# Kernel optimization log

Measured on AMD Instinct MI355X. Metric: run time of the kernel, lower is better.

## Reference

```python
import jax, jax.numpy as jnp
import numpy as np

B, S, D = 8, 2048, 2048
E, R, K = 8, 16, 2
NUM_TASKS, NUM_MODES = 4, 2
ALPHA = 16.0


def setup_inputs() -> dict:
    key = jax.random.key(0)
    k1, k2, k3, k4 = jax.random.split(key, 4)
    hidden_states = jax.random.normal(k1, (B, S, D), dtype=jnp.float32)
    gate_w = jax.random.normal(k2, (E, D), dtype=jnp.float32) * 0.01  # nn.init.normal_(std=0.01)
    # Soft-prior biases: fill(-1.0), strong prior 3.0 / 2.0 at configured (task, expert) / (mode, expert)
    tb = -np.ones((NUM_TASKS, E), dtype=np.float32)
    mb = -np.ones((NUM_MODES, E), dtype=np.float32)
    for e in range(E):
        tb[e % NUM_TASKS, e] = 3.0
        mb[e % NUM_MODES, e] = 2.0
    # LoRA params; lora_B is zero-init in torch but we use small random values for a nontrivial baseline
    lora_A = jax.random.normal(k3, (E, R, D), dtype=jnp.float32) * (1.0 / np.sqrt(D))
    lora_B = jax.random.normal(k4, (E, D, R), dtype=jnp.float32) * 0.02
    return {
        "hidden_states": hidden_states,
        "gate_w": gate_w,
        "task_bias": jnp.asarray(tb),
        "mode_bias": jnp.asarray(mb),
        "lora_A": lora_A,
        "lora_B": lora_B,
        "task_id": 1,
        "mode_id": 1,
    }


def reference(hidden_states, gate_w, task_bias, mode_bias, lora_A, lora_B, task_id, mode_id):
    scaling = ALPHA / R
    # Router: score = dynamic_gate(mean_pool(x)) + task_bias[t] + mode_bias[m]
    x_pooled = hidden_states.mean(axis=1)                       # [B, D]
    logits = x_pooled @ gate_w.T + task_bias[task_id] + mode_bias[mode_id]  # [B, E]
    top_v, top_i = jax.lax.top_k(logits, K)                     # [B, K]
    weights = jax.nn.softmax(top_v, axis=-1)                    # [B, K]
    # per-sample, per-expert combine weight: sum of top-k weights routed to that expert
    one_hot = jax.nn.one_hot(top_i, E, dtype=weights.dtype)     # [B, K, E]
    sw = jnp.einsum('bke,bk->be', one_hot, weights)             # [B, E]
    # LoRA experts: (x @ A_e^T) @ B_e^T * scaling, weighted-summed per sample
    mid = jnp.einsum('bsd,erd->besr', hidden_states, lora_A)    # [B, E, S, R] (small: R=16)
    out = jnp.einsum('be,besr,edr->bsd', sw, mid, lora_B) * scaling  # [B, S, D]
    return out
```

## Files before the change

### kernel.cpp

```cpp
#include <hip/hip_runtime.h>
#include <stdint.h>

typedef __attribute__((ext_vector_type(8))) short bf16x8;
typedef __attribute__((ext_vector_type(4))) float f32x4;
typedef __attribute__((ext_vector_type(16))) float f32x16;
typedef unsigned short ushort_t;

#define B_ 8
#define S_ 2048
#define D_ 2048
#define E_ 8
#define J_ 128
#define M_ 32
#define AROWS 136
#define ATILE (AROWS * 64)

static __device__ __forceinline__ unsigned short f2bf(float f) {
  union { float f; uint32_t u; } v; v.f = f;
  uint32_t u = v.u;
  return (unsigned short)((u + 0x7FFFu + ((u >> 16) & 1u)) >> 16);
}
static __device__ __forceinline__ float bf2f(ushort_t h) {
  union { uint32_t u; float f; } v; v.u = ((uint32_t)h) << 16;
  return v.f;
}
static __device__ __forceinline__ uint32_t pkbf(float a, float b) {
  uint32_t r;
  asm("v_cvt_pk_bf16_f32 %0, %1, %2" : "=v"(r) : "v"(a), "v"(b));
  return r;
}

#define GLL16(gsrc, ldst)                                                        \
  __builtin_amdgcn_global_load_lds(                                              \
      (const __attribute__((address_space(1))) void*)(gsrc),                     \
      (__attribute__((address_space(3))) void*)(ldst), 16, 0, 0)

#define SBAR() __builtin_amdgcn_sched_barrier(0)
#define VMWAIT(N)                                                                \
  do {                                                                           \
    asm volatile("s_waitcnt vmcnt(" #N ")" ::: "memory");                        \
    __builtin_amdgcn_sched_barrier(0);                                           \
  } while (0)
#define VMBAR(N)                                                                 \
  do {                                                                           \
    asm volatile("s_waitcnt vmcnt(" #N ") lgkmcnt(0)\n\ts_barrier" ::: "memory");\
    __builtin_amdgcn_sched_barrier(0);                                           \
  } while (0)

__global__ void k_prep(const float* __restrict__ lA, const float* __restrict__ lB,
                       const float* __restrict__ gw,
                       ushort_t* __restrict__ AgE, ushort_t* __restrict__ Bg) {
  int gid = blockIdx.x * blockDim.x + threadIdx.x;
  int stride = gridDim.x * blockDim.x;
  for (int o = gid; o < 32 * AROWS * 8; o += stride) {
    int kt = o / (AROWS * 8);
    int rem = o - kt * (AROWS * 8);
    int row = rem >> 3, c = rem & 7;
    int d = kt * 64 + (((c ^ row) & 7) << 3);
    const float* src = (row < 128) ? (lA + (size_t)row * D_ + d)
                                   : (gw + (size_t)(row - 128) * D_ + d);
    float4 v0 = *(const float4*)src;
    float4 v1 = *(const float4*)(src + 4);
    bf16x8 outv;
    outv[0] = (short)f2bf(v0.x); outv[1] = (short)f2bf(v0.y);
    outv[2] = (short)f2bf(v0.z); outv[3] = (short)f2bf(v0.w);
    outv[4] = (short)f2bf(v1.x); outv[5] = (short)f2bf(v1.y);
    outv[6] = (short)f2bf(v1.z); outv[7] = (short)f2bf(v1.w);
    *(bf16x8*)&AgE[(size_t)o * 8] = outv;
  }
  for (int o4 = gid; o4 < (D_ * J_) / 4; o4 += stride) {
    int j4 = o4 & 31, dd = o4 >> 5;
    int e = j4 >> 2, r0 = (j4 & 3) * 4;
    float4 v = *(const float4*)(lB + ((size_t)e * D_ + dd) * 16 + r0);
    uint2 pk;
    pk.x = (uint32_t)f2bf(v.x) | ((uint32_t)f2bf(v.y) << 16);
    pk.y = (uint32_t)f2bf(v.z) | ((uint32_t)f2bf(v.w) << 16);
    ((uint2*)Bg)[o4] = pk;
  }
}

__global__ __launch_bounds__(256, 2) void k_mid(const float* __restrict__ x,
    const ushort_t* __restrict__ AgE, ushort_t* __restrict__ midb,
    float* __restrict__ lpart) {
  __shared__ ushort_t Ab[3][ATILE];
  __shared__ ushort_t Xb[2][M_ * 64];
  const int tid = threadIdx.x;
  const int w = tid >> 6, lane = tid & 63;
  const int l31 = lane & 31, hi = lane >> 5;
  const int jp = w & 1, xi = w >> 1;
  const int b = blockIdx.y, s0 = blockIdx.x * M_;
  const int xr = tid >> 3, xc = (tid & 7) * 8;
  const float* xsrc = x + ((size_t)(b * S_ + s0 + xr)) * D_ + xc;
  const int xwoff = xr * 64 + (((tid & 7) ^ (xr & 7)) << 3);

  f32x16 accA = {}, accB = {}, acc2 = {};

  auto stageA = [&](int buf, int kt) {
#pragma unroll
    for (int c = 0; c < 4; ++c) {
      int ch = c * 256 + tid;
      GLL16(AgE + (size_t)kt * ATILE + (size_t)ch * 8, &Ab[buf][ch * 8]);
    }
    {
      int ch = 1024 + lane;
      GLL16(AgE + (size_t)kt * ATILE + (size_t)ch * 8, &Ab[buf][(1024 + lane) * 8]);
    }
  };
  auto loadX = [&](float4* r4, int t) {
    const float* p = xsrc + t * 64;
    r4[0] = *(const float4*)(p);
    r4[1] = *(const float4*)(p + 4);
  };
  auto cvtWrite = [&](int buf, const float4* r4) {
    uint4 q;
    q.x = pkbf(r4[0].x, r4[0].y); q.y = pkbf(r4[0].z, r4[0].w);
    q.z = pkbf(r4[1].x, r4[1].y); q.w = pkbf(r4[1].z, r4[1].w);
    *(uint4*)&Xb[buf][xwoff] = q;
  };
  auto computeTile = [&](int t, int ab) {
    const int xbuf = t & 1;
    const int a0 = jp * 64 + l31, a1 = jp * 64 + 32 + l31, a2 = 128 + l31;
    const int rsw = (l31 & 7);
#pragma unroll
    for (int k2 = 0; k2 < 2; ++k2) {
      const int ks = xi * 2 + k2;
      const int cc = ks * 2 + hi;
      const int chs = ((cc ^ rsw) << 3);
      bf16x8 xf = *(const bf16x8*)&Xb[xbuf][l31 * 64 + chs];
      bf16x8 af0 = *(const bf16x8*)&Ab[ab][a0 * 64 + chs];
      bf16x8 af1 = *(const bf16x8*)&Ab[ab][a1 * 64 + chs];
      accA = __builtin_amdgcn_mfma_f32_32x32x16_bf16(af0, xf, accA, 0, 0, 0);
      accB = __builtin_amdgcn_mfma_f32_32x32x16_bf16(af1, xf, accB, 0, 0, 0);
      if (jp == 0) {
        bf16x8 af2 = *(const bf16x8*)&Ab[ab][a2 * 64 + chs];
        acc2 = __builtin_amdgcn_mfma_f32_32x32x16_bf16(af2, xf, acc2, 0, 0, 0);
      }
    }
  };

  float4 xS0[2], xS1[2];
  loadX(xS0, 0); SBAR();
  stageA(0, 0);  SBAR();
  loadX(xS1, 1); SBAR();
  stageA(1, 1);  SBAR();
  VMWAIT(12);
  cvtWrite(0, xS0);
  VMBAR(7);

#define BODY(T, AB, ABN, XCUR, XNXT)                                             \
  do {                                                                           \
    loadX(XNXT, (T) + 2); SBAR();                                                \
    stageA((ABN), (T) + 2); SBAR();                                              \
    computeTile((T), (AB));                                                      \
    VMWAIT(12);                                                                  \
    cvtWrite(((T) + 1) & 1, XCUR);                                               \
    VMBAR(7);                                                                    \
  } while (0)

#pragma unroll 1
  for (int k6 = 0; k6 < 5; ++k6) {
    const int t0 = 6 * k6;
    BODY(t0 + 0, 0, 2, xS1, xS0);
    BODY(t0 + 1, 1, 0, xS0, xS1);
    BODY(t0 + 2, 2, 1, xS1, xS0);
    BODY(t0 + 3, 0, 2, xS0, xS1);
    BODY(t0 + 4, 1, 0, xS1, xS0);
    BODY(t0 + 5, 2, 1, xS0, xS1);
  }
#undef BODY
  computeTile(30, 0);
  VMWAIT(5);
  cvtWrite(1, xS1);
  VMBAR(0);
  computeTile(31, 1);

  __syncthreads();
  float* scr  = (float*)&Ab[0][0];
  float* scr2 = (float*)&Ab[1][0];
  if (xi == 1) {
    float* p = scr + ((size_t)(jp * 64 + lane)) * 32;
#pragma unroll
    for (int G = 0; G < 4; ++G) {
      f32x4 tA, tB;
      tA[0] = accA[G * 4 + 0]; tA[1] = accA[G * 4 + 1];
      tA[2] = accA[G * 4 + 2]; tA[3] = accA[G * 4 + 3];
      tB[0] = accB[G * 4 + 0]; tB[1] = accB[G * 4 + 1];
      tB[2] = accB[G * 4 + 2]; tB[3] = accB[G * 4 + 3];
      *(f32x4*)&p[G * 4]      = tA;
      *(f32x4*)&p[16 + G * 4] = tB;
    }
    if (jp == 0) {
      float* p2 = scr2 + lane * 4;
      p2[0] = acc2[0]; p2[1] = acc2[1]; p2[2] = acc2[2]; p2[3] = acc2[3];
    }
  }
  __syncthreads();
  if (xi == 0) {
    const float* p = scr + ((size_t)(jp * 64 + lane)) * 32;
#pragma unroll
    for (int i = 0; i < 16; ++i) { accA[i] += p[i]; accB[i] += p[16 + i]; }
    ushort_t* mp = midb + ((size_t)(b * S_ + s0 + l31)) * J_ + jp * 64 + 4 * hi;
#pragma unroll
    for (int G = 0; G < 4; ++G) {
      uint2 pA, pB;
      pA.x = pkbf(accA[G * 4 + 0], accA[G * 4 + 1]);
      pA.y = pkbf(accA[G * 4 + 2], accA[G * 4 + 3]);
      pB.x = pkbf(accB[G * 4 + 0], accB[G * 4 + 1]);
      pB.y = pkbf(accB[G * 4 + 2], accB[G * 4 + 3]);
      *(uint2*)&mp[G * 8] = pA;
      *(uint2*)&mp[32 + G * 8] = pB;
    }
    if (jp == 0) {
      const float* p2 = scr2 + lane * 4;
#pragma unroll
      for (int q = 0; q < 4; ++q) {
        float v = acc2[q] + p2[q];
        v += __shfl_xor(v, 1); v += __shfl_xor(v, 2);
        v += __shfl_xor(v, 4); v += __shfl_xor(v, 8);
        v += __shfl_xor(v, 16);
        if (l31 == 0)
          lpart[((size_t)(b * 64 + blockIdx.x)) * 8 + hi * 4 + q] = v;
      }
    }
  }
}

__global__ void k_router(const float* __restrict__ lpart,
                         const float* __restrict__ tb, const float* __restrict__ mb,
                         const int* __restrict__ task_p, const int* __restrict__ mode_p,
                         float* __restrict__ rinfo) {
  __shared__ float lg[64];
  const int t = threadIdx.x;
  const int b = t >> 3, e = t & 7;
  float s = 0.f;
  for (int k = 0; k < 64; ++k) s += lpart[((size_t)(b * 64 + k)) * 8 + e];
  lg[t] = s * (1.f / (float)S_) + tb[task_p[0] * E_ + e] + mb[mode_p[0] * E_ + e];
  __syncthreads();
  if (t < B_) {
    float v[8];
#pragma unroll
    for (int e2 = 0; e2 < 8; ++e2) v[e2] = lg[t * 8 + e2];
    int i1 = 0;
#pragma unroll
    for (int e2 = 1; e2 < 8; ++e2) if (v[e2] > v[i1]) i1 = e2;
    int i2 = (i1 == 0) ? 1 : 0;
#pragma unroll
    for (int e2 = 0; e2 < 8; ++e2) if (e2 != i1 && v[e2] > v[i2]) i2 = e2;
    float ex = __expf(v[i2] - v[i1]);
    float w1 = 1.f / (1.f + ex), w2 = ex * w1;
    float4 r;
    r.x = (float)i1; r.y = (float)i2; r.z = w1; r.w = w2;
    ((float4*)rinfo)[t] = r;
  }
}

__global__ __launch_bounds__(256) void k_comb(const ushort_t* __restrict__ midb,
    const float* __restrict__ rinfo, const ushort_t* __restrict__ Bg,
    float* __restrict__ out) {
  __shared__ ushort_t Bt[128][40];
  const int n = blockIdx.x, m = blockIdx.y, b = blockIdx.z;
  const int tid = threadIdx.x, w = tid >> 6, lane = tid & 63;
  const int lm = lane & 15, g = lane >> 4;

  const float4 ri = ((const float4*)rinfo)[b];
  const int i1 = (int)ri.x, i2 = (int)ri.y;
  const float w1 = ri.z, w2 = ri.w;

#pragma unroll
  for (int c = 0; c < 2; ++c) {
    int ci = c * 256 + tid;
    int d = ci >> 2, sub = ci & 3;
    int e = (sub & 2) ? i2 : i1;
    float sc = (sub & 2) ? w2 : w1;
    bf16x8 bv = *(const bf16x8*)(Bg + ((size_t)(n * 128 + d)) * J_ + e * 16 + (sub & 1) * 8);
    bf16x8 bw;
#pragma unroll
    for (int i = 0; i < 8; ++i) bw[i] = (short)f2bf(bf2f((ushort_t)bv[i]) * sc);
    *(bf16x8*)&Bt[d][sub * 8] = bw;
  }

  const int srow = m * 64 + w * 16 + lm;
  const int jw = (g < 2) ? (i1 * 16 + g * 8) : (i2 * 16 + (g - 2) * 8);
  bf16x8 pf = *(const bf16x8*)&midb[((size_t)(b * S_ + srow)) * J_ + jw];
  __syncthreads();

  f32x4 acc[8] = {};
#pragma unroll
  for (int nn = 0; nn < 8; ++nn) {
    bf16x8 af = *(const bf16x8*)&Bt[nn * 16 + lm][g * 8];
    acc[nn] = __builtin_amdgcn_mfma_f32_16x16x32_bf16(af, pf, acc[nn], 0, 0, 0);
  }

  float* op = out + ((size_t)(b * S_ + srow)) * D_ + n * 128;
#pragma unroll
  for (int nn = 0; nn < 8; ++nn)
    *(f32x4*)&op[nn * 16 + g * 4] = acc[nn];
}

extern "C" void kernel_launch(void* const* d_in, const int* in_sizes, int n_in,
                              void* d_out, int out_size, void* d_ws, size_t ws_size,
                              hipStream_t stream) {
  const float* x    = (const float*)d_in[0];
  const float* gw   = (const float*)d_in[1];
  const float* tb   = (const float*)d_in[2];
  const float* mb   = (const float*)d_in[3];
  const float* lA   = (const float*)d_in[4];
  const float* lB   = (const float*)d_in[5];
  const int* task_p = (const int*)d_in[6];
  const int* mode_p = (const int*)d_in[7];
  float* out = (float*)d_out;
  char* ws = (char*)d_ws;
  ushort_t* midb = (ushort_t*)ws;
  ushort_t* AgE  = (ushort_t*)(ws + 4194304);
  ushort_t* Bg   = (ushort_t*)(ws + 4751360);
  float* lpart   = (float*)(ws + 5275648);
  float* rinfo   = (float*)(ws + 5292032);

  hipLaunchKernelGGL(k_prep, dim3(256), dim3(256), 0, stream, lA, lB, gw, AgE, Bg);
  hipLaunchKernelGGL(k_mid, dim3(64, 8), dim3(256), 0, stream, x, AgE, midb, lpart);
  hipLaunchKernelGGL(k_router, dim3(1), dim3(64), 0, stream,
                     lpart, tb, mb, task_p, mode_p, rinfo);
  hipLaunchKernelGGL(k_comb, dim3(16, 32, 8), dim3(256), 0, stream, midb, rinfo, Bg, out);
}
```

Measured before the change: 84.20 us.

## Double k_mid row tile to 64 with 512-thread blocks and 4-way K split

The mid-projection kernel now handles 64 sequence rows per block using 8 waves. Each wave computes a 2x2 grid of MFMA tiles, so every A-fragment load from LDS is reused across two X fragments, and the four K-slices are reduced through LDS in three rounds. The X tile swizzle is changed to suit the larger tile. Block count is halved, to 256 blocks, which cuts repeated staging of the LoRA-A and gate tiles. In exchange it adds more accumulator registers, a longer serialized reduction, and fewer blocks to spread across the CUs.

New measurement: 76.57 us. 9.1% less time.

```diff
diff --git a/kernel.cpp b/kernel.cpp
--- a/kernel.cpp
+++ b/kernel.cpp
@@ -11,7 +11,7 @@
 #define D_ 2048
 #define E_ 8
 #define J_ 128
-#define M_ 32
+#define M_ 64
 #define AROWS 136
 #define ATILE (AROWS * 64)
 
@@ -28,6 +28,9 @@
   uint32_t r;
   asm("v_cvt_pk_bf16_f32 %0, %1, %2" : "=v"(r) : "v"(a), "v"(b));
   return r;
+}
+static __device__ __forceinline__ int xswz(int row) {
+  return (row & 7) ^ (((row >> 3) & 3) << 1);
 }
 
 #define GLL16(gsrc, ldst)                                                        \
@@ -56,7 +59,7 @@
     int kt = o / (AROWS * 8);
     int rem = o - kt * (AROWS * 8);
     int row = rem >> 3, c = rem & 7;
-    int d = kt * 64 + (((c ^ row) & 7) << 3);
+    int d = kt * 64 + (((c ^ xswz(row)) & 7) << 3);
     const float* src = (row < 128) ? (lA + (size_t)row * D_ + d)
                                    : (gw + (size_t)(row - 128) * D_ + d);
     float4 v0 = *(const float4*)src;
@@ -79,32 +82,29 @@
   }
 }
 
-__global__ __launch_bounds__(256, 2) void k_mid(const float* __restrict__ x,
+__global__ __launch_bounds__(512, 2) void k_mid(const float* __restrict__ x,
     const ushort_t* __restrict__ AgE, ushort_t* __restrict__ midb,
     float* __restrict__ lpart) {
   __shared__ ushort_t Ab[3][ATILE];
-  __shared__ ushort_t Xb[2][M_ * 64];
+  __shared__ ushort_t Xb[2][4096];
+  __shared__ float lsc[4][8];
   const int tid = threadIdx.x;
   const int w = tid >> 6, lane = tid & 63;
   const int l31 = lane & 31, hi = lane >> 5;
-  const int jp = w & 1, xi = w >> 1;
+  const int jp = w & 1, xk = w >> 1;
   const int b = blockIdx.y, s0 = blockIdx.x * M_;
-  const int xr = tid >> 3, xc = (tid & 7) * 8;
-  const float* xsrc = x + ((size_t)(b * S_ + s0 + xr)) * D_ + xc;
-  const int xwoff = xr * 64 + (((tid & 7) ^ (xr & 7)) << 3);
-
-  f32x16 accA = {}, accB = {}, acc2 = {};
+  const int xr = tid >> 3;
+  const float* xsrc = x + ((size_t)(b * S_ + s0 + xr)) * D_ + (tid & 7) * 8;
+  const int xwoff = xr * 64 + ((((tid & 7) ^ xswz(xr)) & 7) << 3);
+  const int Xs = xswz(l31);
+
+  f32x16 acc00 = {}, acc01 = {}, acc10 = {}, acc11 = {}, acc2 = {};
 
   auto stageA = [&](int buf, int kt) {
-#pragma unroll
-    for (int c = 0; c < 4; ++c) {
-      int ch = c * 256 + tid;
-      GLL16(AgE + (size_t)kt * ATILE + (size_t)ch * 8, &Ab[buf][ch * 8]);
-    }
-    {
-      int ch = 1024 + lane;
-      GLL16(AgE + (size_t)kt * ATILE + (size_t)ch * 8, &Ab[buf][(1024 + lane) * 8]);
-    }
+    const ushort_t* base = AgE + (size_t)kt * ATILE;
+    GLL16(base + (size_t)tid * 8, &Ab[buf][tid * 8]);
+    GLL16(base + (size_t)(512 + tid) * 8, &Ab[buf][(512 + tid) * 8]);
+    GLL16(base + (size_t)(1024 + lane) * 8, &Ab[buf][(1024 + lane) * 8]);
   };
   auto loadX = [&](float4* r4, int t) {
     const float* p = xsrc + t * 64;
@@ -118,23 +118,22 @@
     *(uint4*)&Xb[buf][xwoff] = q;
   };
   auto computeTile = [&](int t, int ab) {
-    const int xbuf = t & 1;
-    const int a0 = jp * 64 + l31, a1 = jp * 64 + 32 + l31, a2 = 128 + l31;
-    const int rsw = (l31 & 7);
-#pragma unroll
-    for (int k2 = 0; k2 < 2; ++k2) {
-      const int ks = xi * 2 + k2;
-      const int cc = ks * 2 + hi;
-      const int chs = ((cc ^ rsw) << 3);
-      bf16x8 xf = *(const bf16x8*)&Xb[xbuf][l31 * 64 + chs];
-      bf16x8 af0 = *(const bf16x8*)&Ab[ab][a0 * 64 + chs];
-      bf16x8 af1 = *(const bf16x8*)&Ab[ab][a1 * 64 + chs];
-      accA = __builtin_amdgcn_mfma_f32_32x32x16_bf16(af0, xf, accA, 0, 0, 0);
-      accB = __builtin_amdgcn_mfma_f32_32x32x16_bf16(af1, xf, accB, 0, 0, 0);
-      if (jp == 0) {
-        bf16x8 af2 = *(const bf16x8*)&Ab[ab][a2 * 64 + chs];
-        acc2 = __builtin_amdgcn_mfma_f32_32x32x16_bf16(af2, xf, acc2, 0, 0, 0);
-      }
+    const int cc = xk * 2 + hi;
+    const int chs = (((cc ^ Xs) & 7) << 3);
+    const ushort_t* Xp = &Xb[t & 1][l31 * 64 + chs];
+    bf16x8 xf0 = *(const bf16x8*)Xp;
+    bf16x8 xf1 = *(const bf16x8*)(Xp + 2048);
+    const ushort_t* Ap = &Ab[ab][(jp * 64 + l31) * 64 + chs];
+    bf16x8 af0 = *(const bf16x8*)Ap;
+    bf16x8 af1 = *(const bf16x8*)(Ap + 2048);
+    acc00 = __builtin_amdgcn_mfma_f32_32x32x16_bf16(af0, xf0, acc00, 0, 0, 0);
+    acc10 = __builtin_amdgcn_mfma_f32_32x32x16_bf16(af0, xf1, acc10, 0, 0, 0);
+    acc01 = __builtin_amdgcn_mfma_f32_32x32x16_bf16(af1, xf0, acc01, 0, 0, 0);
+    acc11 = __builtin_amdgcn_mfma_f32_32x32x16_bf16(af1, xf1, acc11, 0, 0, 0);
+    if (jp == 0) {
+      bf16x8 af2 = *(const bf16x8*)&Ab[ab][(128 + l31) * 64 + chs];
+      acc2 = __builtin_amdgcn_mfma_f32_32x32x16_bf16(af2, xf0, acc2, 0, 0, 0);
+      acc2 = __builtin_amdgcn_mfma_f32_32x32x16_bf16(af2, xf1, acc2, 0, 0, 0);
     }
   };
 
@@ -143,18 +142,18 @@
   stageA(0, 0);  SBAR();
   loadX(xS1, 1); SBAR();
   stageA(1, 1);  SBAR();
-  VMWAIT(12);
+  VMWAIT(8);
   cvtWrite(0, xS0);
-  VMBAR(7);
+  VMBAR(5);
 
 #define BODY(T, AB, ABN, XCUR, XNXT)                                             \
   do {                                                                           \
     loadX(XNXT, (T) + 2); SBAR();                                                \
     stageA((ABN), (T) + 2); SBAR();                                              \
     computeTile((T), (AB));                                                      \
-    VMWAIT(12);                                                                  \
+    VMWAIT(8);                                                                   \
     cvtWrite(((T) + 1) & 1, XCUR);                                               \
-    VMBAR(7);                                                                    \
+    VMBAR(5);                                                                    \
   } while (0)
 
 #pragma unroll 1
@@ -169,59 +168,78 @@
   }
 #undef BODY
   computeTile(30, 0);
-  VMWAIT(5);
+  VMWAIT(3);
   cvtWrite(1, xS1);
   VMBAR(0);
   computeTile(31, 1);
 
   __syncthreads();
-  float* scr  = (float*)&Ab[0][0];
-  float* scr2 = (float*)&Ab[1][0];
-  if (xi == 1) {
-    float* p = scr + ((size_t)(jp * 64 + lane)) * 32;
-#pragma unroll
-    for (int G = 0; G < 4; ++G) {
-      f32x4 tA, tB;
-      tA[0] = accA[G * 4 + 0]; tA[1] = accA[G * 4 + 1];
-      tA[2] = accA[G * 4 + 2]; tA[3] = accA[G * 4 + 3];
-      tB[0] = accB[G * 4 + 0]; tB[1] = accB[G * 4 + 1];
-      tB[2] = accB[G * 4 + 2]; tB[3] = accB[G * 4 + 3];
-      *(f32x4*)&p[G * 4]      = tA;
-      *(f32x4*)&p[16 + G * 4] = tB;
-    }
-    if (jp == 0) {
-      float* p2 = scr2 + lane * 4;
-      p2[0] = acc2[0]; p2[1] = acc2[1]; p2[2] = acc2[2]; p2[3] = acc2[3];
+
+  if (jp == 0) {
+#pragma unroll
+    for (int q = 0; q < 4; ++q) {
+      float v = acc2[q];
+      v += __shfl_xor(v, 1); v += __shfl_xor(v, 2); v += __shfl_xor(v, 4);
+      v += __shfl_xor(v, 8); v += __shfl_xor(v, 16);
+      if (l31 == 0) lsc[xk][hi * 4 + q] = v;
+    }
+  }
+
+  float* const reg0 = (float*)&Ab[0][0];
+  float* const reg1 = (float*)&Ab[1][0];
+#pragma unroll 1
+  for (int r = 1; r <= 3; ++r) {
+    __syncthreads();
+    if (xk == r) {
+      float* p = jp ? reg1 : reg0;
+#pragma unroll
+      for (int i = 0; i < 16; ++i) {
+        p[i * 64 + lane]        = acc00[i];
+        p[(16 + i) * 64 + lane] = acc01[i];
+        p[(32 + i) * 64 + lane] = acc10[i];
+        p[(48 + i) * 64 + lane] = acc11[i];
+      }
+    }
+    __syncthreads();
+    if (xk == 0) {
+      const float* p = jp ? reg1 : reg0;
+#pragma unroll
+      for (int i = 0; i < 16; ++i) {
+        acc00[i] += p[i * 64 + lane];
+        acc01[i] += p[(16 + i) * 64 + lane];
+        acc10[i] += p[(32 + i) * 64 + lane];
+        acc11[i] += p[(48 + i) * 64 + lane];
+      }
     }
   }
   __syncthreads();
-  if (xi == 0) {
-    const float* p = scr + ((size_t)(jp * 64 + lane)) * 32;
-#pragma unroll
-    for (int i = 0; i < 16; ++i) { accA[i] += p[i]; accB[i] += p[16 + i]; }
-    ushort_t* mp = midb + ((size_t)(b * S_ + s0 + l31)) * J_ + jp * 64 + 4 * hi;
-#pragma unroll
-    for (int G = 0; G < 4; ++G) {
-      uint2 pA, pB;
-      pA.x = pkbf(accA[G * 4 + 0], accA[G * 4 + 1]);
-      pA.y = pkbf(accA[G * 4 + 2], accA[G * 4 + 3]);
-      pB.x = pkbf(accB[G * 4 + 0], accB[G * 4 + 1]);
-      pB.y = pkbf(accB[G * 4 + 2], accB[G * 4 + 3]);
-      *(uint2*)&mp[G * 8] = pA;
-      *(uint2*)&mp[32 + G * 8] = pB;
-    }
-    if (jp == 0) {
-      const float* p2 = scr2 + lane * 4;
-#pragma unroll
-      for (int q = 0; q < 4; ++q) {
-        float v = acc2[q] + p2[q];
-        v += __shfl_xor(v, 1); v += __shfl_xor(v, 2);
-        v += __shfl_xor(v, 4); v += __shfl_xor(v, 8);
-        v += __shfl_xor(v, 16);
-        if (l31 == 0)
-          lpart[((size_t)(b * 64 + blockIdx.x)) * 8 + hi * 4 + q] = v;
+
+  if (xk == 0) {
+#pragma unroll
+    for (int sp = 0; sp < 2; ++sp) {
+      ushort_t* mp = midb + ((size_t)(b * S_ + s0 + sp * 32 + l31)) * J_ + jp * 64 + 4 * hi;
+#pragma unroll
+      for (int G = 0; G < 4; ++G) {
+        uint2 pA, pB;
+        if (sp == 0) {
+          pA.x = pkbf(acc00[G * 4 + 0], acc00[G * 4 + 1]);
+          pA.y = pkbf(acc00[G * 4 + 2], acc00[G * 4 + 3]);
+          pB.x = pkbf(acc01[G * 4 + 0], acc01[G * 4 + 1]);
+          pB.y = pkbf(acc01[G * 4 + 2], acc01[G * 4 + 3]);
+        } else {
+          pA.x = pkbf(acc10[G * 4 + 0], acc10[G * 4 + 1]);
+          pA.y = pkbf(acc10[G * 4 + 2], acc10[G * 4 + 3]);
+          pB.x = pkbf(acc11[G * 4 + 0], acc11[G * 4 + 1]);
+          pB.y = pkbf(acc11[G * 4 + 2], acc11[G * 4 + 3]);
+        }
+        *(uint2*)&mp[G * 8] = pA;
+        *(uint2*)&mp[32 + G * 8] = pB;
       }
     }
+  }
+  if (w == 0 && lane < 8) {
+    float s = lsc[0][lane] + lsc[1][lane] + lsc[2][lane] + lsc[3][lane];
+    lpart[((size_t)(b * 32 + blockIdx.x)) * 8 + lane] = s;
   }
 }
 
@@ -233,7 +251,7 @@
   const int t = threadIdx.x;
   const int b = t >> 3, e = t & 7;
   float s = 0.f;
-  for (int k = 0; k < 64; ++k) s += lpart[((size_t)(b * 64 + k)) * 8 + e];
+  for (int k = 0; k < 32; ++k) s += lpart[((size_t)(b * 32 + k)) * 8 + e];
   lg[t] = s * (1.f / (float)S_) + tb[task_p[0] * E_ + e] + mb[mode_p[0] * E_ + e];
   __syncthreads();
   if (t < B_) {
@@ -314,10 +332,10 @@
   ushort_t* AgE  = (ushort_t*)(ws + 4194304);
   ushort_t* Bg   = (ushort_t*)(ws + 4751360);
   float* lpart   = (float*)(ws + 5275648);
-  float* rinfo   = (float*)(ws + 5292032);
+  float* rinfo   = (float*)(ws + 5283840);
 
   hipLaunchKernelGGL(k_prep, dim3(256), dim3(256), 0, stream, lA, lB, gw, AgE, Bg);
-  hipLaunchKernelGGL(k_mid, dim3(64, 8), dim3(256), 0, stream, x, AgE, midb, lpart);
+  hipLaunchKernelGGL(k_mid, dim3(32, 8), dim3(512), 0, stream, x, AgE, midb, lpart);
   hipLaunchKernelGGL(k_router, dim3(1), dim3(64), 0, stream,
                      lpart, tb, mb, task_p, mode_p, rinfo);
   hipLaunchKernelGGL(k_comb, dim3(16, 32, 8), dim3(256), 0, stream, midb, rinfo, Bg, out);
```
